# Kernel optimization log

Hardware: AMD Instinct MI355X
Metric: run time of the kernel (lower is better)

Reference implementation:

```python
import jax, jax.numpy as jnp
import numpy as np

B, F, D_IN, H, OUT = 32768, 200, 5, 15, 30

def setup_inputs() -> dict:
    key = jax.random.key(0)
    ks = jax.random.split(key, 7)
    return {
        "y":  jax.random.normal(ks[0], (B, F, D_IN), dtype=jnp.float32),
        "W1": jax.random.normal(ks[1], (F, D_IN, H), dtype=jnp.float32) * 0.3,
        "b1": jax.random.normal(ks[2], (F, H), dtype=jnp.float32) * 0.1,
        "W2": jax.random.normal(ks[3], (F, H, OUT), dtype=jnp.float32) * 0.2,
        "b2": jax.random.normal(ks[4], (F, OUT), dtype=jnp.float32) * 0.1,
        "W3": jax.random.normal(ks[5], (F * OUT, 1), dtype=jnp.float32) * 0.02,
        "b3": jax.random.normal(ks[6], (1,), dtype=jnp.float32) * 0.1,
    }

def reference(y, W1, b1, W2, b2, W3, b3):
    # 200 independent tiny 2-layer MLPs, batched over the feature axis f.
    # Note: original applies ReLU only AFTER the second Linear.
    h1 = jnp.einsum('bfi,fih->bfh', y, W1) + b1          # [B, F, H]
    h2 = jax.nn.relu(jnp.einsum('bfh,fho->bfo', h1, W2) + b2)  # [B, F, OUT]
    flat = h2.reshape(h2.shape[0], -1)                   # concat along feature axis -> [B, F*OUT]
    return flat @ W3 + b3                                # [B, 1]
```

## Files before the change

kernel.cpp:

```cpp
#include <hip/hip_runtime.h>

#define B_TOTAL 32768
#define NF 200
#define D_IN 5
#define NH 15
#define NOUT 30

typedef _Float16 half8 __attribute__((ext_vector_type(8)));
typedef _Float16 half4_t __attribute__((ext_vector_type(4)));
typedef float f32x4 __attribute__((ext_vector_type(4)));

#define WS_BC_BYTES 102400
#define WS_TOTAL (102400 + 30720)

#define GPF 8

__global__ __launch_bounds__(256) void precompute_kernel(
    const float* __restrict__ W1, const float* __restrict__ b1,
    const float* __restrict__ W2, const float* __restrict__ b2,
    const float* __restrict__ W3, _Float16* __restrict__ Bc,
    float* __restrict__ w3T, float* __restrict__ out)
{
    __shared__ __align__(16) float sW1[GPF * 75];
    __shared__ __align__(16) float sW2[GPF * 450];
    __shared__ __align__(16) float sb1[GPF * 15];
    __shared__ __align__(16) float sb2[GPF * 30];
    __shared__ __align__(16) float sW3[GPF * 30];

    const int tid = threadIdx.x;
    const int f0  = blockIdx.x * GPF;

    {
        const f32x4 z4 = {0.f, 0.f, 0.f, 0.f};
        for (int j = blockIdx.x * 256 + tid; j < B_TOTAL / 4; j += 25 * 256)
            ((f32x4*)out)[j] = z4;
    }

    {
        const f32x4* g1 = (const f32x4*)(W1 + (size_t)f0 * 75);
        if (tid < 150) ((f32x4*)sW1)[tid] = g1[tid];
        const f32x4* g2 = (const f32x4*)(W2 + (size_t)f0 * 450);
        for (int j = tid; j < 900; j += 256) ((f32x4*)sW2)[j] = g2[j];
        if (tid < 30)
            ((f32x4*)sb1)[tid] = ((const f32x4*)(b1 + (size_t)f0 * 15))[tid];
        if (tid >= 32 && tid < 92)
            ((f32x4*)sb2)[tid - 32] = ((const f32x4*)(b2 + (size_t)f0 * 30))[tid - 32];
        if (tid >= 96 && tid < 156)
            ((f32x4*)sW3)[tid - 96] = ((const f32x4*)(W3 + (size_t)f0 * 30))[tid - 96];
    }
    __syncthreads();

    const int fi = tid >> 5;
    const int r  = tid & 31;
    const int hf = r >> 4;
    const int n  = r & 15;
    const int o  = hf * 16 + n;
    const int f  = f0 + fi;

    half8 row = {};
    if (o < NOUT) {
        float bcv = sb2[fi * 30 + o];
        float wc0 = 0.f, wc1 = 0.f, wc2 = 0.f, wc3 = 0.f, wc4 = 0.f;
        #pragma unroll
        for (int h = 0; h < NH; ++h) {
            const float w2v = sW2[fi * 450 + h * 30 + o];
            bcv = fmaf(sb1[fi * 15 + h], w2v, bcv);
            wc0 = fmaf(sW1[fi * 75 +  0 + h], w2v, wc0);
            wc1 = fmaf(sW1[fi * 75 + 15 + h], w2v, wc1);
            wc2 = fmaf(sW1[fi * 75 + 30 + h], w2v, wc2);
            wc3 = fmaf(sW1[fi * 75 + 45 + h], w2v, wc3);
            wc4 = fmaf(sW1[fi * 75 + 60 + h], w2v, wc4);
        }
        row[0] = (_Float16)wc0; row[1] = (_Float16)wc1; row[2] = (_Float16)wc2;
        row[3] = (_Float16)wc3; row[4] = (_Float16)wc4;
        row[5] = (_Float16)bcv;
        row[6] = (_Float16)0.f; row[7] = (_Float16)0.f;

        const int p = f / 20, fl = f % 20, Kg = fl / 4, w = fl % 4;
        w3T[((size_t)(p * 4 + w) * 16 + n) * 12 + (Kg * 2 + hf)] = sW3[fi * 30 + o];
    }
    *(half8*)(Bc + (size_t)f * 256 + r * 8) = row;
}

#define FPART 20
#define NPARTS 10

__global__ __launch_bounds__(256, 4) void mlp_kernel(
    const float* __restrict__ y, const _Float16* __restrict__ Bc,
    const float* __restrict__ w3T, const float* __restrict__ b3,
    float* __restrict__ out)
{
    __shared__ __align__(16) _Float16 sy[64 * 168];
    __shared__ __align__(16) _Float16 sB[20 * 256];
    __shared__ __align__(16) float    sw3[4 * 16 * 12];
    __shared__ __align__(16) _Float16 szero[8];

    const int tid = threadIdx.x;
    const int b0  = blockIdx.x * 64;
    const int p   = blockIdx.y;
    const int f0  = p * FPART;

    if (tid < 8) szero[tid] = (_Float16)0.f;
    {
        const f32x4* g = (const f32x4*)(Bc + (size_t)f0 * 256);
        f32x4* s = (f32x4*)sB;
        s[tid]       = g[tid];
        s[tid + 256] = g[tid + 256];
        if (tid < 128) s[tid + 512] = g[tid + 512];
    }
    if (tid < 192) ((f32x4*)sw3)[tid] = ((const f32x4*)w3T)[(size_t)p * 192 + tid];
    #pragma unroll
    for (int it = 0; it < 5; ++it) {
        const int id = tid + it * 256;
        const int b  = id / 20;
        const int fl = id - b * 20;
        const float* src = y + (size_t)(b0 + b) * (NF * D_IN) + (size_t)(f0 + fl) * 5;
        float v[5];
        __builtin_memcpy(v, src, 20);
        half8 h;
        h[0] = (_Float16)v[0]; h[1] = (_Float16)v[1]; h[2] = (_Float16)v[2];
        h[3] = (_Float16)v[3]; h[4] = (_Float16)v[4];
        h[5] = (_Float16)1.0f; h[6] = (_Float16)0.f; h[7] = (_Float16)0.f;
        *(half8*)&sy[b * 168 + fl * 8] = h;
    }
    __syncthreads();

    const int lane = tid & 63;
    const int w    = tid >> 6;
    const int n    = lane & 15;
    const int q    = lane >> 4;

    float acc[4][4];
    #pragma unroll
    for (int Mt = 0; Mt < 4; ++Mt)
        #pragma unroll
        for (int g = 0; g < 4; ++g) acc[Mt][g] = 0.f;

    #pragma unroll 1
    for (int Kg = 0; Kg < 5; ++Kg) {
        const int fl = Kg * 4 + w;
        half8 A[4];
        #pragma unroll
        for (int Mt = 0; Mt < 4; ++Mt)
            A[Mt] = *(const half8*)&sy[(Mt * 16 + n) * 168 + (Kg * 4 + q) * 8];

        const _Float16* bp0 = (q == w) ? &sB[fl * 256 + n * 8]        : szero;
        const _Float16* bp1 = (q == w) ? &sB[fl * 256 + (16 + n) * 8] : szero;
        const half8 Bf0 = *(const half8*)bp0;
        const half8 Bf1 = *(const half8*)bp1;

        const float* w3p = &sw3[(w * 16 + n) * 12 + Kg * 2];
        const float w30 = w3p[0], w31 = w3p[1];

        #pragma unroll
        for (int Mt = 0; Mt < 4; ++Mt) {
            f32x4 c0 = {0.f, 0.f, 0.f, 0.f};
            f32x4 c1 = {0.f, 0.f, 0.f, 0.f};
            c0 = __builtin_amdgcn_mfma_f32_16x16x32_f16(A[Mt], Bf0, c0, 0, 0, 0);
            c1 = __builtin_amdgcn_mfma_f32_16x16x32_f16(A[Mt], Bf1, c1, 0, 0, 0);
            #pragma unroll
            for (int g = 0; g < 4; ++g)
                acc[Mt][g] += fmaxf(c0[g], 0.f) * w30 + fmaxf(c1[g], 0.f) * w31;
        }
    }

    #pragma unroll
    for (int Mt = 0; Mt < 4; ++Mt)
        #pragma unroll
        for (int g = 0; g < 4; ++g) {
            float v = acc[Mt][g];
            v += __shfl_xor(v, 1, 16);
            v += __shfl_xor(v, 2, 16);
            v += __shfl_xor(v, 4, 16);
            v += __shfl_xor(v, 8, 16);
            acc[Mt][g] = v;
        }
    if (n == 0) {
        #pragma unroll
        for (int Mt = 0; Mt < 4; ++Mt)
            #pragma unroll
            for (int g = 0; g < 4; ++g) {
                const int b = b0 + Mt * 16 + q * 4 + g;
                float v = acc[Mt][g];
                if (p == 0 && w == 0) v += b3[0];
                atomicAdd(&out[b], v);
            }
    }
}

extern "C" void kernel_launch(void* const* d_in, const int* in_sizes, int n_in,
                              void* d_out, int out_size, void* d_ws, size_t ws_size,
                              hipStream_t stream) {
    const float* y  = (const float*)d_in[0];
    const float* W1 = (const float*)d_in[1];
    const float* b1 = (const float*)d_in[2];
    const float* W2 = (const float*)d_in[3];
    const float* b2 = (const float*)d_in[4];
    const float* W3 = (const float*)d_in[5];
    const float* b3 = (const float*)d_in[6];
    float* out = (float*)d_out;

    _Float16* Bc  = (_Float16*)d_ws;
    float*    w3T = (float*)((char*)d_ws + WS_BC_BYTES);

    precompute_kernel<<<NF / GPF, 256, 0, stream>>>(W1, b1, W2, b2, W3, Bc, w3T, out);
    mlp_kernel<<<dim3(B_TOTAL / 64, NPARTS), 256, 0, stream>>>(y, Bc, w3T, b3, out);
}
```

Baseline: 212.7 us.

## Use 16x16x16 MFMA with half-width fragments and LDS-based block reduction

Switches the per-feature MFMA from 16x16x32 (which wasted three quarters of K on zero blocks) to 16x16x16 with half4 fragments. Lanes with q>=2 feed zeros, so each wave computes only its own feature. The cross-lane shuffle reduction and the 16 atomics per wave are replaced by an LDS transpose and sum across the four waves, leaving one atomicAdd per batch row per block. This adds two __syncthreads and reuses the sy/sB buffers as scratch.

```diff
diff --git a/kernel.cpp b/kernel.cpp
--- a/kernel.cpp
+++ b/kernel.cpp
@@ -9,6 +9,7 @@
 typedef _Float16 half8 __attribute__((ext_vector_type(8)));
 typedef _Float16 half4_t __attribute__((ext_vector_type(4)));
 typedef float f32x4 __attribute__((ext_vector_type(4)));
+typedef float f32x2 __attribute__((ext_vector_type(2)));
 
 #define WS_BC_BYTES 102400
 #define WS_TOTAL (102400 + 30720)
@@ -135,56 +136,60 @@
     for (int Mt = 0; Mt < 4; ++Mt)
         #pragma unroll
         for (int g = 0; g < 4; ++g) acc[Mt][g] = 0.f;
+    const f32x4 z4 = {0.f, 0.f, 0.f, 0.f};
 
     #pragma unroll 1
     for (int Kg = 0; Kg < 5; ++Kg) {
         const int fl = Kg * 4 + w;
-        half8 A[4];
+        half4_t A[4];
         #pragma unroll
         for (int Mt = 0; Mt < 4; ++Mt)
-            A[Mt] = *(const half8*)&sy[(Mt * 16 + n) * 168 + (Kg * 4 + q) * 8];
-
-        const _Float16* bp0 = (q == w) ? &sB[fl * 256 + n * 8]        : szero;
-        const _Float16* bp1 = (q == w) ? &sB[fl * 256 + (16 + n) * 8] : szero;
-        const half8 Bf0 = *(const half8*)bp0;
-        const half8 Bf1 = *(const half8*)bp1;
-
-        const float* w3p = &sw3[(w * 16 + n) * 12 + Kg * 2];
+            A[Mt] = *(const half4_t*)&sy[(Mt * 16 + n) * 168 + fl * 8 + (q & 1) * 4];
+
+        const _Float16* bq0 = (q < 2) ? &sB[fl * 256 + n * 8 + (q & 1) * 4]        : szero;
+        const _Float16* bq1 = (q < 2) ? &sB[fl * 256 + (16 + n) * 8 + (q & 1) * 4] : szero;
+        const half4_t Bf0 = *(const half4_t*)bq0;
+        const half4_t Bf1 = *(const half4_t*)bq1;
+
+        const f32x2 w3p = *(const f32x2*)&sw3[(w * 16 + n) * 12 + Kg * 2];
         const float w30 = w3p[0], w31 = w3p[1];
 
         #pragma unroll
         for (int Mt = 0; Mt < 4; ++Mt) {
-            f32x4 c0 = {0.f, 0.f, 0.f, 0.f};
-            f32x4 c1 = {0.f, 0.f, 0.f, 0.f};
-            c0 = __builtin_amdgcn_mfma_f32_16x16x32_f16(A[Mt], Bf0, c0, 0, 0, 0);
-            c1 = __builtin_amdgcn_mfma_f32_16x16x32_f16(A[Mt], Bf1, c1, 0, 0, 0);
+            f32x4 c0 = __builtin_amdgcn_mfma_f32_16x16x16f16(A[Mt], Bf0, z4, 0, 0, 0);
+            f32x4 c1 = __builtin_amdgcn_mfma_f32_16x16x16f16(A[Mt], Bf1, z4, 0, 0, 0);
             #pragma unroll
             for (int g = 0; g < 4; ++g)
                 acc[Mt][g] += fmaxf(c0[g], 0.f) * w30 + fmaxf(c1[g], 0.f) * w31;
         }
     }
 
-    #pragma unroll
-    for (int Mt = 0; Mt < 4; ++Mt)
-        #pragma unroll
-        for (int g = 0; g < 4; ++g) {
-            float v = acc[Mt][g];
-            v += __shfl_xor(v, 1, 16);
-            v += __shfl_xor(v, 2, 16);
-            v += __shfl_xor(v, 4, 16);
-            v += __shfl_xor(v, 8, 16);
-            acc[Mt][g] = v;
-        }
-    if (n == 0) {
+    __syncthreads();
+    float* sacc = (float*)sy;
+    {
+        float* base = sacc + w * (64 * 20);
         #pragma unroll
         for (int Mt = 0; Mt < 4; ++Mt)
             #pragma unroll
-            for (int g = 0; g < 4; ++g) {
-                const int b = b0 + Mt * 16 + q * 4 + g;
-                float v = acc[Mt][g];
-                if (p == 0 && w == 0) v += b3[0];
-                atomicAdd(&out[b], v);
-            }
+            for (int g = 0; g < 4; ++g)
+                base[(Mt * 16 + q * 4 + g) * 20 + n] = acc[Mt][g];
+    }
+    const float* srow = sacc + w * (64 * 20) + lane * 20;
+    f32x4 r0 = *(const f32x4*)(srow);
+    f32x4 r1 = *(const f32x4*)(srow + 4);
+    f32x4 r2 = *(const f32x4*)(srow + 8);
+    f32x4 r3 = *(const f32x4*)(srow + 12);
+    float v = ((r0[0] + r0[1]) + (r0[2] + r0[3]))
+            + ((r1[0] + r1[1]) + (r1[2] + r1[3]))
+            + ((r2[0] + r2[1]) + (r2[2] + r2[3]))
+            + ((r3[0] + r3[1]) + (r3[2] + r3[3]));
+    float* sp = (float*)sB;
+    sp[w * 64 + lane] = v;
+    __syncthreads();
+    if (tid < 64) {
+        float s = (sp[tid] + sp[64 + tid]) + (sp[128 + tid] + sp[192 + tid]);
+        if (p == 0) s += b3[0];
+        atomicAdd(&out[b0 + tid], s);
     }
 }
 
```

New measurement: 208.6 us, median of 2. No clear change (-1.9%).
